# Kernel tuning notes

Hardware: AMD Instinct MI355X
Metric: run time of the kernel (lower is better)

Reference implementation:

```python
import jax, jax.numpy as jnp
import numpy as np

B, S, E, H = 2, 2048, 2048, 16
D = E // H  # head_out == qk_out (linformer_factor=1, attention_groups=0)
NEG = -1e30


def alibi_slopes(n_heads):
    # standard ALiBi slopes: 2^(-8*h/n_heads) for h = 1..n_heads
    return jnp.asarray(2.0 ** (-8.0 * np.arange(1, n_heads + 1) / n_heads), dtype=jnp.float32)


def setup_inputs() -> dict:
    key = jax.random.key(0)
    ks = jax.random.split(key, 5)
    sc = 0.02
    return {
        "x": jax.random.normal(ks[0], (B, S, E), dtype=jnp.float32),
        "Wq": jax.random.normal(ks[1], (E, E), dtype=jnp.float32) * sc,
        "Wk": jax.random.normal(ks[2], (E, E), dtype=jnp.float32) * sc,
        "Wv": jax.random.normal(ks[3], (E, E), dtype=jnp.float32) * sc,
        "Wo": jax.random.normal(ks[4], (E, E), dtype=jnp.float32) * sc,
        "bo": jnp.zeros((E,), dtype=jnp.float32),
    }


def reference(x, Wq, Wk, Wv, Wo, bo):
    b, s, e = x.shape
    # projections, split heads: [b, H, s, D]
    q = (x @ Wq).reshape(b, s, H, D).transpose(0, 2, 1, 3)
    k = (x @ Wk).reshape(b, s, H, D).transpose(0, 2, 1, 3)
    v = (x @ Wv).reshape(b, s, H, D).transpose(0, 2, 1, 3)
    scores = jnp.einsum("bhqd,bhkd->bhqk", q, k)
    # causal mask applied BEFORE scaling (as in original calc_attention)
    i = jnp.arange(s)[:, None]
    j = jnp.arange(s)[None, :]
    causal = j <= i  # [s, s]
    scores = jnp.where(causal[None, None], scores, NEG)
    # ALiBi bias: slope_h * (j - i), added before scaling
    bias = alibi_slopes(H)[:, None, None] * (j - i).astype(jnp.float32)  # [H, s, s]
    scores = scores + bias[None]
    scores = scores / jnp.sqrt(jnp.float32(D))
    w = jax.nn.softmax(scores, axis=-1)  # dropout rate 0.0 -> identity
    ctx = jnp.einsum("bhqk,bhkd->bqhd", w, v).reshape(b, s, e)
    return ctx @ Wo + bo
```

## Files before the change

kernel.cpp:

```cpp
#include <hip/hip_runtime.h>

#define BB 2
#define SS 2048
#define EE 2048
#define HH 16
#define DD 128
#define SE (3 * EE)

typedef __bf16 bf16x8 __attribute__((ext_vector_type(8)));
typedef unsigned short u16x8 __attribute__((ext_vector_type(8)));
typedef float f32x4 __attribute__((ext_vector_type(4)));

__device__ __forceinline__ unsigned short f32_to_bf16(float f) {
  unsigned int u = __builtin_bit_cast(unsigned int, f);
  u += 0x7FFFu + ((u >> 16) & 1u);
  return (unsigned short)(u >> 16);
}

__device__ __forceinline__ void gll16(const void* g, const void* lds) {
  __builtin_amdgcn_global_load_lds(
      (const __attribute__((address_space(1))) unsigned int*)g,
      (__attribute__((address_space(3))) unsigned int*)lds, 16, 0, 0);
}

__device__ __forceinline__ bf16x8 lds_frag(const unsigned short* p) {
  return __builtin_bit_cast(bf16x8, *(const u16x8*)p);
}

__global__ void k_cast_bf16(const float* __restrict__ x, unsigned short* __restrict__ y) {
  int i = blockIdx.x * 256 + threadIdx.x;
  float4 v = ((const float4*)x)[i];
  ushort4 o;
  o.x = f32_to_bf16(v.x); o.y = f32_to_bf16(v.y);
  o.z = f32_to_bf16(v.z); o.w = f32_to_bf16(v.w);
  ((ushort4*)y)[i] = o;
}

__global__ void k_transpose_w4(const float* __restrict__ W0, const float* __restrict__ W1,
                               const float* __restrict__ W2, const float* __restrict__ W3,
                               unsigned short* __restrict__ WtBase) {
  const float* W = blockIdx.z == 0 ? W0 : blockIdx.z == 1 ? W1 : blockIdx.z == 2 ? W2 : W3;
  unsigned short* Wt = WtBase + (size_t)blockIdx.z * EE * EE;
  __shared__ float tile[32][33];
  int n0 = blockIdx.x * 32, k0 = blockIdx.y * 32;
  int t = threadIdx.x, r = t >> 5, c = t & 31;
  for (int i = 0; i < 32; i += 8)
    tile[r + i][c] = W[(size_t)(k0 + r + i) * EE + n0 + c];
  __syncthreads();
  for (int i = 0; i < 32; i += 8)
    Wt[(size_t)(n0 + r + i) * EE + k0 + c] = f32_to_bf16(tile[c][r + i]);
}

template <int OUTF32>
__global__ __launch_bounds__(256, 4) void k_gemm_bt(
    const unsigned short* __restrict__ A, const unsigned short* __restrict__ Bt,
    void* __restrict__ Cout, const float* __restrict__ bias,
    unsigned short* __restrict__ VtOut, int K, int N) {
  __shared__ unsigned short As[128 * 64];
  __shared__ unsigned short Bs[128 * 64];
  const int tid = threadIdx.x;
  const int l = tid & 63, w = tid >> 6;
  const int m0 = blockIdx.y * 128, n0 = blockIdx.x * 128;
  const int tm = l & 15, qc = l >> 4;
  const int swz = tm & 7;
  const int m_base = (w >> 1) * 64, n_base = (w & 1) * 64;
  f32x4 acc[4][4] = {};

  for (int k0 = 0; k0 < K; k0 += 64) {
    for (int is = 0; is < 4; ++is) {
      int o = (w * 4 + is) * 1024 + l * 16;
      int row = o >> 7, slot = (o >> 4) & 7;
      int c = slot ^ (row & 7);
      gll16(&A[(size_t)(m0 + row) * K + k0 + c * 8], ((const char*)As) + o);
      gll16(&Bt[(size_t)(n0 + row) * K + k0 + c * 8], ((const char*)Bs) + o);
    }
    __syncthreads();
    for (int ks = 0; ks < 2; ++ks) {
      bf16x8 a[4], b[4];
      for (int im = 0; im < 4; ++im)
        a[im] = lds_frag(&As[(m_base + im * 16 + tm) * 64 + (((ks * 4 + qc) ^ swz) << 3)]);
      for (int in = 0; in < 4; ++in)
        b[in] = lds_frag(&Bs[(n_base + in * 16 + tm) * 64 + (((ks * 4 + qc) ^ swz) << 3)]);
      for (int im = 0; im < 4; ++im)
        for (int in = 0; in < 4; ++in)
          acc[im][in] = __builtin_amdgcn_mfma_f32_16x16x32_bf16(a[im], b[in], acc[im][in], 0, 0, 0);
    }
    __syncthreads();
  }

  if (!OUTF32 && n0 >= 2 * EE) {
    for (int im = 0; im < 4; ++im)
      for (int in = 0; in < 4; ++in) {
        int row0 = m0 + m_base + im * 16 + qc * 4;
        int col = n0 + n_base + in * 16 + tm - 2 * EE;
        int b = row0 >> 11, s = row0 & 2047;
        int h = col >> 7, d = col & 127;
        ushort4 o;
        o.x = f32_to_bf16(acc[im][in][0]);
        o.y = f32_to_bf16(acc[im][in][1]);
        o.z = f32_to_bf16(acc[im][in][2]);
        o.w = f32_to_bf16(acc[im][in][3]);
        *(ushort4*)&VtOut[((size_t)((b * HH + h) * DD + d) << 11) + s] = o;
      }
    return;
  }

  for (int im = 0; im < 4; ++im)
    for (int in = 0; in < 4; ++in)
      for (int r = 0; r < 4; ++r) {
        int row = m0 + m_base + im * 16 + (l >> 4) * 4 + r;
        int col = n0 + n_base + in * 16 + tm;
        if (OUTF32)
          ((float*)Cout)[(size_t)row * N + col] = acc[im][in][r] + bias[col];
        else
          ((unsigned short*)Cout)[(size_t)row * N + col] = f32_to_bf16(acc[im][in][r]);
      }
}

__global__ __launch_bounds__(256, 2) void k_attn(
    const unsigned short* __restrict__ QKV, const unsigned short* __restrict__ Vt,
    unsigned short* __restrict__ ctx) {
  __shared__ unsigned short smem[40960];
  const int tid = threadIdx.x;
  const int l = tid & 63, w = tid >> 6;
  const int tm = l & 15, qc = l >> 4;
  const int bh = blockIdx.x, b = bh >> 4, h = bh & 15;
  const int rank = blockIdx.y;
  const int t = (rank < 8) ? (15 - rank) : (rank - 8);
  const int q0 = t * 128;
  const int n_it = 2 * t + 2;
  const float c1 = 0.12751676f;
  const float slopeL = exp2f(-0.5f * (float)(h + 1)) * c1;

  const unsigned short* Qg = QKV + h * DD;
  const unsigned short* Kg = QKV + EE + h * DD;
  const unsigned short* Vg = Vt + (size_t)bh * DD * SS;
  unsigned short* Ps = smem + 32768 + w * 2048;

  for (int is = 0; is < 8; ++is) {
    int idx = (w * 8 + is) * 64 + l;
    int row = idx >> 4, c = (idx & 15) ^ (row & 7);
    gll16(&Qg[(size_t)(b * SS + q0 + row) * SE + c * 8], ((char*)smem) + 32768 + idx * 16);
  }
  for (int is = 0; is < 4; ++is) {
    int idx = (w * 4 + is) * 64 + l;
    int kr = idx >> 4, kc = (idx & 15) ^ (kr & 7);
    gll16(&Kg[(size_t)(b * SS + kr) * SE + kc * 8], ((char*)smem) + idx * 16);
    int vr = idx >> 3, vc = (idx & 7) ^ (vr & 7);
    gll16(&Vg[(size_t)vr * SS + vc * 8], ((char*)smem) + 16384 + idx * 16);
  }
  __syncthreads();
  bf16x8 qf[2][4];
  for (int im = 0; im < 2; ++im)
    for (int kk = 0; kk < 4; ++kk) {
      int row = w * 32 + im * 16 + tm;
      qf[im][kk] = lds_frag(&smem[16384 + (row * 16 + ((kk * 4 + qc) ^ (tm & 7))) * 8]);
    }
  __syncthreads();

  float lr[2][4] = {};
  f32x4 o[2][8] = {};

  for (int it = 0; it < n_it; ++it) {
    const int kt = it * 64;
    const unsigned short* K_ = smem + (it & 1) * 16384;
    const unsigned short* V_ = K_ + 8192;
    if (it + 1 < n_it) {
      char* Kd = ((char*)smem) + ((it + 1) & 1) * 32768;
      int ktn = kt + 64;
      for (int is = 0; is < 4; ++is) {
        int idx = (w * 4 + is) * 64 + l;
        int kr = idx >> 4, kc = (idx & 15) ^ (kr & 7);
        gll16(&Kg[(size_t)(b * SS + ktn + kr) * SE + kc * 8], Kd + idx * 16);
        int vr = idx >> 3, vc = (idx & 7) ^ (vr & 7);
        gll16(&Vg[(size_t)vr * SS + ktn + vc * 8], Kd + 16384 + idx * 16);
      }
    }
    const bool full = (kt + 64 <= q0);

    for (int kn = 0; kn < 4; ++kn) {
      bf16x8 kf[4];
      for (int kk = 0; kk < 4; ++kk) {
        int row = kn * 16 + tm;
        kf[kk] = lds_frag(&K_[(row * 16 + ((kk * 4 + qc) ^ (tm & 7))) * 8]);
      }
      f32x4 a0 = {}, a1 = {};
      for (int kk = 0; kk < 4; ++kk) {
        a0 = __builtin_amdgcn_mfma_f32_16x16x32_bf16(qf[0][kk], kf[kk], a0, 0, 0, 0);
        a1 = __builtin_amdgcn_mfma_f32_16x16x32_bf16(qf[1][kk], kf[kk], a1, 0, 0, 0);
      }
      const int j = kt + kn * 16 + tm;
      for (int im = 0; im < 2; ++im) {
        const f32x4 av = im ? a1 : a0;
        const int ibase = q0 + w * 32 + im * 16 + qc * 4;
        for (int r = 0; r < 4; ++r) {
          int d = j - (ibase + r);
          float arg = av[r] * c1 + slopeL * (float)d;
          if (!full && d > 0) arg = -1e30f;
          float p = __builtin_amdgcn_exp2f(arg);
          lr[im][r] += p;
          unsigned int u = __builtin_bit_cast(unsigned int, p);
          int prow = im * 16 + qc * 4 + r;
          int pslot = (kn * 2 + (tm >> 3)) ^ (prow & 7);
          Ps[(prow * 8 + pslot) * 8 + (tm & 7)] = (unsigned short)(u >> 16);
        }
      }
    }
    asm volatile("s_waitcnt lgkmcnt(0)" ::: "memory");
    bf16x8 pf[2][2];
    for (int im = 0; im < 2; ++im)
      for (int k2 = 0; k2 < 2; ++k2) {
        int prow = im * 16 + tm;
        pf[im][k2] = lds_frag(&Ps[(prow * 8 + ((k2 * 4 + qc) ^ (tm & 7))) * 8]);
      }
    for (int dc = 0; dc < 8; ++dc) {
      int vrow = dc * 16 + tm;
      bf16x8 vf0 = lds_frag(&V_[(vrow * 8 + (qc ^ (tm & 7))) * 8]);
      bf16x8 vf1 = lds_frag(&V_[(vrow * 8 + ((4 + qc) ^ (tm & 7))) * 8]);
      o[0][dc] = __builtin_amdgcn_mfma_f32_16x16x32_bf16(pf[0][0], vf0, o[0][dc], 0, 0, 0);
      o[0][dc] = __builtin_amdgcn_mfma_f32_16x16x32_bf16(pf[0][1], vf1, o[0][dc], 0, 0, 0);
      o[1][dc] = __builtin_amdgcn_mfma_f32_16x16x32_bf16(pf[1][0], vf0, o[1][dc], 0, 0, 0);
      o[1][dc] = __builtin_amdgcn_mfma_f32_16x16x32_bf16(pf[1][1], vf1, o[1][dc], 0, 0, 0);
    }
    __syncthreads();
  }

  for (int im = 0; im < 2; ++im)
    for (int r = 0; r < 4; ++r) {
      float s = lr[im][r];
      for (int off = 8; off >= 1; off >>= 1) s += __shfl_xor(s, off, 64);
      float inv = 1.0f / s;
      int i = q0 + w * 32 + im * 16 + qc * 4 + r;
      for (int dc = 0; dc < 8; ++dc)
        ctx[(size_t)(b * SS + i) * EE + h * DD + dc * 16 + tm] =
            f32_to_bf16(o[im][dc][r] * inv);
    }
}

extern "C" void kernel_launch(void* const* d_in, const int* in_sizes, int n_in,
                              void* d_out, int out_size, void* d_ws, size_t ws_size,
                              hipStream_t stream) {
  const float* x  = (const float*)d_in[0];
  const float* Wq = (const float*)d_in[1];
  const float* Wk = (const float*)d_in[2];
  const float* Wv = (const float*)d_in[3];
  const float* Wo = (const float*)d_in[4];
  const float* bo = (const float*)d_in[5];
  float* out = (float*)d_out;

  const size_t XE = (size_t)BB * SS * EE;
  const size_t WE = (size_t)EE * EE;
  unsigned short* ws   = (unsigned short*)d_ws;
  unsigned short* xb   = ws;
  unsigned short* WqT  = xb + XE;
  unsigned short* WoT  = WqT + 3 * WE;
  unsigned short* QKVb = WoT + WE;
  unsigned short* Vt   = QKVb + 3 * XE;
  unsigned short* ctx  = xb;

  k_cast_bf16<<<XE / 1024, 256, 0, stream>>>(x, xb);
  k_transpose_w4<<<dim3(EE / 32, EE / 32, 4), 256, 0, stream>>>(Wq, Wk, Wv, Wo, WqT);

  dim3 gqkv(SE / 128, (BB * SS) / 128);
  k_gemm_bt<0><<<gqkv, 256, 0, stream>>>(xb, WqT, QKVb, nullptr, Vt, EE, SE);

  k_attn<<<dim3(BB * HH, SS / 128), 256, 0, stream>>>(QKVb, Vt, ctx);

  dim3 gg(EE / 128, (BB * SS) / 128);
  k_gemm_bt<1><<<gg, 256, 0, stream>>>(ctx, WoT, out, bo, nullptr, EE, EE);
}
```

Measured before the change: 342.0 us.

## Keep softmax probabilities in registers by transposing attention MFMAs

Swaps MFMA operand order so the score tile comes out transposed (keys along rows per lane). The exponentiated probabilities can then be packed directly into bf16 B-operand fragments with v_cvt_pk_bf16_f32, with no round trip through a per-wave LDS scratch buffer. The PV product is likewise transposed, with V fragments gathered as two 8-byte LDS reads, and the output is written as 4-wide vector stores. This removes LDS writes and reads plus the lgkmcnt wait, and shrinks shared memory, in exchange for split 64-bit V loads and a different bf16 rounding path for P.

```diff
diff --git a/kernel.cpp b/kernel.cpp
--- a/kernel.cpp
+++ b/kernel.cpp
@@ -10,11 +10,19 @@
 typedef __bf16 bf16x8 __attribute__((ext_vector_type(8)));
 typedef unsigned short u16x8 __attribute__((ext_vector_type(8)));
 typedef float f32x4 __attribute__((ext_vector_type(4)));
+typedef unsigned long long u64;
+typedef u64 u64x2 __attribute__((ext_vector_type(2)));
 
 __device__ __forceinline__ unsigned short f32_to_bf16(float f) {
   unsigned int u = __builtin_bit_cast(unsigned int, f);
   u += 0x7FFFu + ((u >> 16) & 1u);
   return (unsigned short)(u >> 16);
+}
+
+__device__ __forceinline__ unsigned int cvt_pk_bf16(float lo, float hi) {
+  unsigned int r;
+  asm("v_cvt_pk_bf16_f32 %0, %1, %2" : "=v"(r) : "v"(lo), "v"(hi));
+  return r;
 }
 
 __device__ __forceinline__ void gll16(const void* g, const void* lds) {
@@ -120,7 +128,7 @@
 __global__ __launch_bounds__(256, 2) void k_attn(
     const unsigned short* __restrict__ QKV, const unsigned short* __restrict__ Vt,
     unsigned short* __restrict__ ctx) {
-  __shared__ unsigned short smem[40960];
+  __shared__ unsigned short smem[32768];
   const int tid = threadIdx.x;
   const int l = tid & 63, w = tid >> 6;
   const int tm = l & 15, qc = l >> 4;
@@ -135,7 +143,6 @@
   const unsigned short* Qg = QKV + h * DD;
   const unsigned short* Kg = QKV + EE + h * DD;
   const unsigned short* Vg = Vt + (size_t)bh * DD * SS;
-  unsigned short* Ps = smem + 32768 + w * 2048;
 
   for (int is = 0; is < 8; ++is) {
     int idx = (w * 8 + is) * 64 + l;
@@ -158,8 +165,9 @@
     }
   __syncthreads();
 
-  float lr[2][4] = {};
+  float lr[2] = {};
   f32x4 o[2][8] = {};
+  const int qA = q0 + w * 32 + tm;
 
   for (int it = 0; it < n_it; ++it) {
     const int kt = it * 64;
@@ -178,63 +186,80 @@
     }
     const bool full = (kt + 64 <= q0);
 
+    unsigned int pfu[2][2][4];
+#pragma unroll
     for (int kn = 0; kn < 4; ++kn) {
       bf16x8 kf[4];
+#pragma unroll
       for (int kk = 0; kk < 4; ++kk) {
         int row = kn * 16 + tm;
         kf[kk] = lds_frag(&K_[(row * 16 + ((kk * 4 + qc) ^ (tm & 7))) * 8]);
       }
       f32x4 a0 = {}, a1 = {};
+#pragma unroll
       for (int kk = 0; kk < 4; ++kk) {
-        a0 = __builtin_amdgcn_mfma_f32_16x16x32_bf16(qf[0][kk], kf[kk], a0, 0, 0, 0);
-        a1 = __builtin_amdgcn_mfma_f32_16x16x32_bf16(qf[1][kk], kf[kk], a1, 0, 0, 0);
-      }
-      const int j = kt + kn * 16 + tm;
+        a0 = __builtin_amdgcn_mfma_f32_16x16x32_bf16(kf[kk], qf[0][kk], a0, 0, 0, 0);
+        a1 = __builtin_amdgcn_mfma_f32_16x16x32_bf16(kf[kk], qf[1][kk], a1, 0, 0, 0);
+      }
+      const int jb = kt + kn * 16 + qc * 4;
+#pragma unroll
       for (int im = 0; im < 2; ++im) {
         const f32x4 av = im ? a1 : a0;
-        const int ibase = q0 + w * 32 + im * 16 + qc * 4;
+        const int dbase = jb - (qA + im * 16);
+        const float fb = slopeL * (float)dbase;
+        float p[4];
+#pragma unroll
         for (int r = 0; r < 4; ++r) {
-          int d = j - (ibase + r);
-          float arg = av[r] * c1 + slopeL * (float)d;
-          if (!full && d > 0) arg = -1e30f;
-          float p = __builtin_amdgcn_exp2f(arg);
-          lr[im][r] += p;
-          unsigned int u = __builtin_bit_cast(unsigned int, p);
-          int prow = im * 16 + qc * 4 + r;
-          int pslot = (kn * 2 + (tm >> 3)) ^ (prow & 7);
-          Ps[(prow * 8 + pslot) * 8 + (tm & 7)] = (unsigned short)(u >> 16);
+          float arg = av[r] * c1 + (fb + slopeL * (float)r);
+          if (!full && dbase + r > 0) arg = -1e30f;
+          p[r] = __builtin_amdgcn_exp2f(arg);
         }
-      }
-    }
-    asm volatile("s_waitcnt lgkmcnt(0)" ::: "memory");
+        lr[im] += (p[0] + p[1]) + (p[2] + p[3]);
+        pfu[im][kn >> 1][(kn & 1) * 2]     = cvt_pk_bf16(p[0], p[1]);
+        pfu[im][kn >> 1][(kn & 1) * 2 + 1] = cvt_pk_bf16(p[2], p[3]);
+      }
+    }
     bf16x8 pf[2][2];
+#pragma unroll
     for (int im = 0; im < 2; ++im)
+#pragma unroll
+      for (int k2 = 0; k2 < 2; ++k2)
+        pf[im][k2] = __builtin_bit_cast(bf16x8, *(unsigned int(*)[4])&pfu[im][k2][0]);
+
+#pragma unroll
+    for (int dc = 0; dc < 8; ++dc) {
+      const int drow = (dc * 16 + tm) * 64;
+      const int hw = (qc & 1) * 4;
+#pragma unroll
       for (int k2 = 0; k2 < 2; ++k2) {
-        int prow = im * 16 + tm;
-        pf[im][k2] = lds_frag(&Ps[(prow * 8 + ((k2 * 4 + qc) ^ (tm & 7))) * 8]);
-      }
+        int sl0 = (k2 * 4 + (qc >> 1)) ^ (tm & 7);
+        int sl1 = (k2 * 4 + 2 + (qc >> 1)) ^ (tm & 7);
+        u64x2 c;
+        c[0] = *(const u64*)&V_[drow + sl0 * 8 + hw];
+        c[1] = *(const u64*)&V_[drow + sl1 * 8 + hw];
+        bf16x8 vfrag = __builtin_bit_cast(bf16x8, c);
+        o[0][dc] = __builtin_amdgcn_mfma_f32_16x16x32_bf16(vfrag, pf[0][k2], o[0][dc], 0, 0, 0);
+        o[1][dc] = __builtin_amdgcn_mfma_f32_16x16x32_bf16(vfrag, pf[1][k2], o[1][dc], 0, 0, 0);
+      }
+    }
+    __syncthreads();
+  }
+
+  for (int im = 0; im < 2; ++im) {
+    float s = lr[im];
+    s += __shfl_xor(s, 16, 64);
+    s += __shfl_xor(s, 32, 64);
+    float inv = 1.0f / s;
+    int q = qA + im * 16;
     for (int dc = 0; dc < 8; ++dc) {
-      int vrow = dc * 16 + tm;
-      bf16x8 vf0 = lds_frag(&V_[(vrow * 8 + (qc ^ (tm & 7))) * 8]);
-      bf16x8 vf1 = lds_frag(&V_[(vrow * 8 + ((4 + qc) ^ (tm & 7))) * 8]);
-      o[0][dc] = __builtin_amdgcn_mfma_f32_16x16x32_bf16(pf[0][0], vf0, o[0][dc], 0, 0, 0);
-      o[0][dc] = __builtin_amdgcn_mfma_f32_16x16x32_bf16(pf[0][1], vf1, o[0][dc], 0, 0, 0);
-      o[1][dc] = __builtin_amdgcn_mfma_f32_16x16x32_bf16(pf[1][0], vf0, o[1][dc], 0, 0, 0);
-      o[1][dc] = __builtin_amdgcn_mfma_f32_16x16x32_bf16(pf[1][1], vf1, o[1][dc], 0, 0, 0);
-    }
-    __syncthreads();
-  }
-
-  for (int im = 0; im < 2; ++im)
-    for (int r = 0; r < 4; ++r) {
-      float s = lr[im][r];
-      for (int off = 8; off >= 1; off >>= 1) s += __shfl_xor(s, off, 64);
-      float inv = 1.0f / s;
-      int i = q0 + w * 32 + im * 16 + qc * 4 + r;
-      for (int dc = 0; dc < 8; ++dc)
-        ctx[(size_t)(b * SS + i) * EE + h * DD + dc * 16 + tm] =
-            f32_to_bf16(o[im][dc][r] * inv);
-    }
+      ushort4 ov;
+      ov.x = f32_to_bf16(o[im][dc][0] * inv);
+      ov.y = f32_to_bf16(o[im][dc][1] * inv);
+      ov.z = f32_to_bf16(o[im][dc][2] * inv);
+      ov.w = f32_to_bf16(o[im][dc][3] * inv);
+      *(ushort4*)&ctx[(size_t)(b * SS + q) * EE + h * DD + dc * 16 + qc * 4] = ov;
+    }
+  }
 }
 
 extern "C" void kernel_launch(void* const* d_in, const int* in_sizes, int n_in,
```

After: 355.0 us. 1.04x slower.

## Shrink attention tiles to 64 queries and 32 keys for higher occupancy

Applied to the files above, without the earlier changes.

The attention kernel now processes 64 query rows per block (16 per wave) with 32-key tiles instead of 128x64. LDS use drops from about 80KB to 36KB and launch bounds rise to 4 blocks per CU, with twice as many blocks and a new four-way causal load-balancing order. The aim is better latency hiding and a finer causal work split. In exchange, each K/V tile loaded from global memory is reused by fewer query rows, and each iteration does less MFMA work relative to its synchronisation.

```diff
diff --git a/kernel.cpp b/kernel.cpp
--- a/kernel.cpp
+++ b/kernel.cpp
@@ -117,17 +117,18 @@
       }
 }
 
-__global__ __launch_bounds__(256, 2) void k_attn(
+__global__ __launch_bounds__(256, 4) void k_attn(
     const unsigned short* __restrict__ QKV, const unsigned short* __restrict__ Vt,
     unsigned short* __restrict__ ctx) {
-  __shared__ unsigned short smem[40960];
+  __shared__ unsigned short smem[18432];
   const int tid = threadIdx.x;
   const int l = tid & 63, w = tid >> 6;
   const int tm = l & 15, qc = l >> 4;
   const int bh = blockIdx.x, b = bh >> 4, h = bh & 15;
   const int rank = blockIdx.y;
-  const int t = (rank < 8) ? (15 - rank) : (rank - 8);
-  const int q0 = t * 128;
+  const int rr = rank & 7, sel = rank >> 3;
+  const int t = (sel == 0) ? rr : (sel == 1) ? 15 - rr : (sel == 2) ? 16 + rr : 31 - rr;
+  const int q0 = t * 64;
   const int n_it = 2 * t + 2;
   const float c1 = 0.12751676f;
   const float slopeL = exp2f(-0.5f * (float)(h + 1)) * c1;
@@ -135,106 +136,96 @@
   const unsigned short* Qg = QKV + h * DD;
   const unsigned short* Kg = QKV + EE + h * DD;
   const unsigned short* Vg = Vt + (size_t)bh * DD * SS;
-  unsigned short* Ps = smem + 32768 + w * 2048;
-
-  for (int is = 0; is < 8; ++is) {
-    int idx = (w * 8 + is) * 64 + l;
-    int row = idx >> 4, c = (idx & 15) ^ (row & 7);
-    gll16(&Qg[(size_t)(b * SS + q0 + row) * SE + c * 8], ((char*)smem) + 32768 + idx * 16);
-  }
+  unsigned short* Ps = smem + 16384 + w * 512;
+
   for (int is = 0; is < 4; ++is) {
     int idx = (w * 4 + is) * 64 + l;
-    int kr = idx >> 4, kc = (idx & 15) ^ (kr & 7);
-    gll16(&Kg[(size_t)(b * SS + kr) * SE + kc * 8], ((char*)smem) + idx * 16);
-    int vr = idx >> 3, vc = (idx & 7) ^ (vr & 7);
-    gll16(&Vg[(size_t)vr * SS + vc * 8], ((char*)smem) + 16384 + idx * 16);
-  }
-  __syncthreads();
-  bf16x8 qf[2][4];
-  for (int im = 0; im < 2; ++im)
-    for (int kk = 0; kk < 4; ++kk) {
-      int row = w * 32 + im * 16 + tm;
-      qf[im][kk] = lds_frag(&smem[16384 + (row * 16 + ((kk * 4 + qc) ^ (tm & 7))) * 8]);
-    }
-  __syncthreads();
-
-  float lr[2][4] = {};
-  f32x4 o[2][8] = {};
+    int row = idx >> 4, c = (idx & 15) ^ (row & 7);
+    gll16(&Qg[(size_t)(b * SS + q0 + row) * SE + c * 8], ((char*)smem) + idx * 16);
+  }
+  __syncthreads();
+  bf16x8 qf[4];
+  {
+    int row = w * 16 + tm;
+    for (int kk = 0; kk < 4; ++kk)
+      qf[kk] = lds_frag(&smem[(row * 16 + ((kk * 4 + qc) ^ (tm & 7))) * 8]);
+  }
+  __syncthreads();
+
+  {
+    char* Kd = (char*)smem;
+    for (int is = 0; is < 2; ++is) {
+      int idx = (w * 2 + is) * 64 + l;
+      int kr = idx >> 4, kc = (idx & 15) ^ (kr & 7);
+      gll16(&Kg[(size_t)(b * SS + kr) * SE + kc * 8], Kd + idx * 16);
+      int vr = idx >> 2, vc = (idx & 3) ^ (vr & 3);
+      gll16(&Vg[(size_t)vr * SS + vc * 8], Kd + 8192 + idx * 16);
+    }
+  }
+  __syncthreads();
+
+  float lr[4] = {};
+  f32x4 o[8] = {};
+  const int ibase0 = q0 + w * 16 + qc * 4;
 
   for (int it = 0; it < n_it; ++it) {
-    const int kt = it * 64;
-    const unsigned short* K_ = smem + (it & 1) * 16384;
-    const unsigned short* V_ = K_ + 8192;
+    const int kt = it * 32;
+    const unsigned short* K_ = smem + (it & 1) * 8192;
+    const unsigned short* V_ = K_ + 4096;
     if (it + 1 < n_it) {
-      char* Kd = ((char*)smem) + ((it + 1) & 1) * 32768;
-      int ktn = kt + 64;
-      for (int is = 0; is < 4; ++is) {
-        int idx = (w * 4 + is) * 64 + l;
+      char* Kd = ((char*)smem) + ((it + 1) & 1) * 16384;
+      const int ktn = kt + 32;
+      for (int is = 0; is < 2; ++is) {
+        int idx = (w * 2 + is) * 64 + l;
         int kr = idx >> 4, kc = (idx & 15) ^ (kr & 7);
         gll16(&Kg[(size_t)(b * SS + ktn + kr) * SE + kc * 8], Kd + idx * 16);
-        int vr = idx >> 3, vc = (idx & 7) ^ (vr & 7);
-        gll16(&Vg[(size_t)vr * SS + ktn + vc * 8], Kd + 16384 + idx * 16);
-      }
-    }
-    const bool full = (kt + 64 <= q0);
-
-    for (int kn = 0; kn < 4; ++kn) {
+        int vr = idx >> 2, vc = (idx & 3) ^ (vr & 3);
+        gll16(&Vg[(size_t)vr * SS + ktn + vc * 8], Kd + 8192 + idx * 16);
+      }
+    }
+    const bool full = (kt + 32 <= q0);
+
+    for (int kn = 0; kn < 2; ++kn) {
       bf16x8 kf[4];
       for (int kk = 0; kk < 4; ++kk) {
         int row = kn * 16 + tm;
         kf[kk] = lds_frag(&K_[(row * 16 + ((kk * 4 + qc) ^ (tm & 7))) * 8]);
       }
-      f32x4 a0 = {}, a1 = {};
-      for (int kk = 0; kk < 4; ++kk) {
-        a0 = __builtin_amdgcn_mfma_f32_16x16x32_bf16(qf[0][kk], kf[kk], a0, 0, 0, 0);
-        a1 = __builtin_amdgcn_mfma_f32_16x16x32_bf16(qf[1][kk], kf[kk], a1, 0, 0, 0);
-      }
+      f32x4 a0 = {};
+      for (int kk = 0; kk < 4; ++kk)
+        a0 = __builtin_amdgcn_mfma_f32_16x16x32_bf16(qf[kk], kf[kk], a0, 0, 0, 0);
       const int j = kt + kn * 16 + tm;
-      for (int im = 0; im < 2; ++im) {
-        const f32x4 av = im ? a1 : a0;
-        const int ibase = q0 + w * 32 + im * 16 + qc * 4;
-        for (int r = 0; r < 4; ++r) {
-          int d = j - (ibase + r);
-          float arg = av[r] * c1 + slopeL * (float)d;
-          if (!full && d > 0) arg = -1e30f;
-          float p = __builtin_amdgcn_exp2f(arg);
-          lr[im][r] += p;
-          unsigned int u = __builtin_bit_cast(unsigned int, p);
-          int prow = im * 16 + qc * 4 + r;
-          int pslot = (kn * 2 + (tm >> 3)) ^ (prow & 7);
-          Ps[(prow * 8 + pslot) * 8 + (tm & 7)] = (unsigned short)(u >> 16);
-        }
+      for (int r = 0; r < 4; ++r) {
+        int d = j - (ibase0 + r);
+        float arg = a0[r] * c1 + slopeL * (float)d;
+        if (!full && d > 0) arg = -1e30f;
+        float p = __builtin_amdgcn_exp2f(arg);
+        lr[r] += p;
+        unsigned int u = __builtin_bit_cast(unsigned int, p);
+        int prow = qc * 4 + r;
+        int pslot = (kn * 2 + (tm >> 3)) ^ (prow & 3);
+        Ps[(prow * 4 + pslot) * 8 + (tm & 7)] = (unsigned short)(u >> 16);
       }
     }
     asm volatile("s_waitcnt lgkmcnt(0)" ::: "memory");
-    bf16x8 pf[2][2];
-    for (int im = 0; im < 2; ++im)
-      for (int k2 = 0; k2 < 2; ++k2) {
-        int prow = im * 16 + tm;
-        pf[im][k2] = lds_frag(&Ps[(prow * 8 + ((k2 * 4 + qc) ^ (tm & 7))) * 8]);
-      }
+    bf16x8 pf = lds_frag(&Ps[(tm * 4 + (qc ^ (tm & 3))) * 8]);
     for (int dc = 0; dc < 8; ++dc) {
       int vrow = dc * 16 + tm;
-      bf16x8 vf0 = lds_frag(&V_[(vrow * 8 + (qc ^ (tm & 7))) * 8]);
-      bf16x8 vf1 = lds_frag(&V_[(vrow * 8 + ((4 + qc) ^ (tm & 7))) * 8]);
-      o[0][dc] = __builtin_amdgcn_mfma_f32_16x16x32_bf16(pf[0][0], vf0, o[0][dc], 0, 0, 0);
-      o[0][dc] = __builtin_amdgcn_mfma_f32_16x16x32_bf16(pf[0][1], vf1, o[0][dc], 0, 0, 0);
-      o[1][dc] = __builtin_amdgcn_mfma_f32_16x16x32_bf16(pf[1][0], vf0, o[1][dc], 0, 0, 0);
-      o[1][dc] = __builtin_amdgcn_mfma_f32_16x16x32_bf16(pf[1][1], vf1, o[1][dc], 0, 0, 0);
+      bf16x8 vf = lds_frag(&V_[(vrow * 4 + (qc ^ (tm & 3))) * 8]);
+      o[dc] = __builtin_amdgcn_mfma_f32_16x16x32_bf16(pf, vf, o[dc], 0, 0, 0);
     }
     __syncthreads();
   }
 
-  for (int im = 0; im < 2; ++im)
-    for (int r = 0; r < 4; ++r) {
-      float s = lr[im][r];
-      for (int off = 8; off >= 1; off >>= 1) s += __shfl_xor(s, off, 64);
-      float inv = 1.0f / s;
-      int i = q0 + w * 32 + im * 16 + qc * 4 + r;
-      for (int dc = 0; dc < 8; ++dc)
-        ctx[(size_t)(b * SS + i) * EE + h * DD + dc * 16 + tm] =
-            f32_to_bf16(o[im][dc][r] * inv);
-    }
+  for (int r = 0; r < 4; ++r) {
+    float s = lr[r];
+    for (int off = 8; off >= 1; off >>= 1) s += __shfl_xor(s, off, 64);
+    float inv = 1.0f / s;
+    int i = ibase0 + r;
+    for (int dc = 0; dc < 8; ++dc)
+      ctx[(size_t)(b * SS + i) * EE + h * DD + dc * 16 + tm] =
+          f32_to_bf16(o[dc][r] * inv);
+  }
 }
 
 extern "C" void kernel_launch(void* const* d_in, const int* in_sizes, int n_in,
@@ -264,7 +255,7 @@
   dim3 gqkv(SE / 128, (BB * SS) / 128);
   k_gemm_bt<0><<<gqkv, 256, 0, stream>>>(xb, WqT, QKVb, nullptr, Vt, EE, SE);
 
-  k_attn<<<dim3(BB * HH, SS / 128), 256, 0, stream>>>(QKVb, Vt, ctx);
+  k_attn<<<dim3(BB * HH, SS / 64), 256, 0, stream>>>(QKVb, Vt, ctx);
 
   dim3 gg(EE / 128, (BB * SS) / 128);
   k_gemm_bt<1><<<gg, 256, 0, stream>>>(ctx, WoT, out, bo, nullptr, EE, EE);
```

Measured after the change: 369.2 us. 1.08x slower.
